# Optimization experiments

Hardware: AMD Instinct MI355X
Metric: run time of the kernel (lower is better)

The kernel has to match this reference:

```python
import jax, jax.numpy as jnp
import numpy as np

IN, H, T = 40, 64, 301


def setup_inputs() -> dict:
    key = jax.random.key(0)
    ks = jax.random.split(key, 7)
    s_ih = 1.0 / np.sqrt(H)
    return {
        "x": jax.random.normal(ks[0], (4096, T, IN), dtype=jnp.float32),
        # PyTorch LSTM layout: gates stacked as [i, f, g, o] along first dim
        "w_ih": jax.random.uniform(ks[1], (4 * H, IN), jnp.float32, -s_ih, s_ih),
        "w_hh": jax.random.uniform(ks[2], (4 * H, H), jnp.float32, -s_ih, s_ih),
        "b_ih": jax.random.uniform(ks[3], (4 * H,), jnp.float32, -s_ih, s_ih),
        "b_hh": jax.random.uniform(ks[4], (4 * H,), jnp.float32, -s_ih, s_ih),
        "w_clf": jax.random.uniform(ks[5], (1, T * H), jnp.float32, -1.0 / np.sqrt(T * H), 1.0 / np.sqrt(T * H)),
        "b_clf": jax.random.uniform(ks[6], (1,), jnp.float32, -1.0 / np.sqrt(T * H), 1.0 / np.sqrt(T * H)),
    }


def _lstm(x, w_ih, w_hh, b_ih, b_hh):
    B = x.shape[0]
    # precompute input projections for all timesteps: [B, T, 4H] -> [T, B, 4H]
    xw = jnp.einsum("bti,gi->btg", x, w_ih) + b_ih + b_hh
    xw = jnp.transpose(xw, (1, 0, 2))

    def step(carry, xt):
        h, c = carry
        z = xt + h @ w_hh.T  # [B, 4H]
        i, f, g, o = jnp.split(z, 4, axis=-1)
        c = jax.nn.sigmoid(f) * c + jax.nn.sigmoid(i) * jnp.tanh(g)
        h = jax.nn.sigmoid(o) * jnp.tanh(c)
        return (h, c), h

    h0 = jnp.zeros((B, H), x.dtype)
    c0 = jnp.zeros((B, H), x.dtype)
    _, hs = jax.lax.scan(step, (h0, c0), xw)  # hs: [T, B, H]
    return jnp.transpose(hs, (1, 0, 2))  # [B, T, H]


def reference(x, w_ih, w_hh, b_ih, b_hh, w_clf, b_clf):
    out = _lstm(x, w_ih, w_hh, b_ih, b_hh)  # [B, T, H]
    flat = out.reshape(out.shape[0], -1)  # [B, T*H]
    return flat @ w_clf.T + b_clf  # [B, 1]
```

## Files before the change

### kernel.cpp

```cpp
#include <hip/hip_runtime.h>

#define T_STEPS 301
#define IN_DIM  40
#define LOG2E   1.44269504088896340736f

typedef __attribute__((ext_vector_type(8))) _Float16 f16x8;
typedef __attribute__((ext_vector_type(4))) float f32x4;
typedef unsigned short ushort_t;
typedef unsigned int uint_t;

__device__ __forceinline__ f16x8 cvt8h(const float4 a, const float4 b) {
  f16x8 r;
  r[0] = (_Float16)a.x; r[1] = (_Float16)a.y; r[2] = (_Float16)a.z; r[3] = (_Float16)a.w;
  r[4] = (_Float16)b.x; r[5] = (_Float16)b.y; r[6] = (_Float16)b.z; r[7] = (_Float16)b.w;
  return r;
}

__device__ __forceinline__ float lstm_act(float zi, float zf, float zg, float zo, float& cc) {
  const float ig = __builtin_amdgcn_rcpf(1.0f + __builtin_amdgcn_exp2f(-zi));
  const float fg = __builtin_amdgcn_rcpf(1.0f + __builtin_amdgcn_exp2f(-zf));
  const float gg = 1.0f - 2.0f * __builtin_amdgcn_rcpf(1.0f + __builtin_amdgcn_exp2f(zg));
  const float og = __builtin_amdgcn_rcpf(1.0f + __builtin_amdgcn_exp2f(-zo));
  cc = fg * cc + ig * gg;
  const float tc = 1.0f - 2.0f * __builtin_amdgcn_rcpf(1.0f + __builtin_amdgcn_exp2f(cc * (2.0f * LOG2E)));
  return og * tc;
}

__global__ __launch_bounds__(256, 2)
void lstm_f16(const float* __restrict__ x, const float* __restrict__ w_ih,
              const float* __restrict__ w_hh, const float* __restrict__ b_ih,
              const float* __restrict__ b_hh, const float* __restrict__ w_clf,
              const float* __restrict__ b_clf, float* __restrict__ out) {
  __shared__ ushort_t hbuf[2][16][64];
  __shared__ float red[64][9];

  const int tid  = threadIdx.x;
  const int l    = tid & 63;
  const int w    = tid >> 6;
  const int arow = l & 15;
  const int g16  = l >> 4;
  const int n    = w * 16 + arow;

  const float gscale[4] = {LOG2E, LOG2E, 2.0f * LOG2E, LOG2E};

  f16x8 whh[4][2], wih[4][2];
  float biasv[4];
#pragma unroll
  for (int c = 0; c < 4; ++c) {
    const float s = gscale[c];
    const float* wr = w_hh + (size_t)(c * 64 + n) * 64;
#pragma unroll
    for (int kc = 0; kc < 2; ++kc) {
      float4 v0 = *(const float4*)(wr + kc * 32 + g16 * 8);
      float4 v1 = *(const float4*)(wr + kc * 32 + g16 * 8 + 4);
      v0.x *= s; v0.y *= s; v0.z *= s; v0.w *= s;
      v1.x *= s; v1.y *= s; v1.z *= s; v1.w *= s;
      whh[c][kc] = cvt8h(v0, v1);
    }
    const float* wir = w_ih + (size_t)(c * 64 + n) * IN_DIM;
    {
      float4 v0 = *(const float4*)(wir + g16 * 8);
      float4 v1 = *(const float4*)(wir + g16 * 8 + 4);
      v0.x *= s; v0.y *= s; v0.z *= s; v0.w *= s;
      v1.x *= s; v1.y *= s; v1.z *= s; v1.w *= s;
      wih[c][0] = cvt8h(v0, v1);
    }
    {
      float4 v0 = make_float4(0, 0, 0, 0), v1 = make_float4(0, 0, 0, 0);
      if (g16 == 0) {
        v0 = *(const float4*)(wir + 32);
        v1 = *(const float4*)(wir + 36);
        v0.x *= s; v0.y *= s; v0.z *= s; v0.w *= s;
        v1.x *= s; v1.y *= s; v1.z *= s; v1.w *= s;
      }
      wih[c][1] = cvt8h(v0, v1);
    }
    biasv[c] = (b_ih[c * 64 + n] + b_hh[c * 64 + n]) * s;
  }

  {
    uint_t* hz = (uint_t*)&hbuf[0][0][0];
    for (int i = tid; i < 1024; i += 256) hz[i] = 0;
  }
  __syncthreads();

  const int slot = ((arow >> 2) << 1) | (arow & 1);
  const int toff = (arow >> 1) & 1;
  const int gb   = blockIdx.x * 8 + slot;
  const float* xbase = x + (size_t)gb * T_STEPS * IN_DIM;

  float4 xa0, xa1, xb0 = make_float4(0, 0, 0, 0), xb1 = make_float4(0, 0, 0, 0);
  {
    const int tm = toff < T_STEPS ? toff : T_STEPS - 1;
    const float* xp = xbase + tm * IN_DIM + g16 * 8;
    xa0 = *(const float4*)xp;
    xa1 = *(const float4*)(xp + 4);
    if (g16 == 0) {
      xb0 = *(const float4*)(xbase + tm * IN_DIM + 32);
      xb1 = *(const float4*)(xbase + tm * IN_DIM + 36);
    }
  }

  f32x4 zacc[4];
  float cc0 = 0.f, cc1 = 0.f, a0 = 0.f, a1 = 0.f;
  float wc_cur = w_clf[n];

  const int row0 = g16 * 4, row1 = row0 + 1;
  const int wo0 = row0 * 64 + ((((n >> 3) ^ (row0 & 7)) << 3) | (n & 7));
  const int wo1 = row1 * 64 + ((((n >> 3) ^ (row1 & 7)) << 3) | (n & 7));
  ushort_t* hflat = &hbuf[0][0][0];

  for (int t = 0; t < T_STEPS; ++t) {
    const int rb = t & 1, wb = rb ^ 1;

    f16x8 ah0, ah1;
    {
      const int cj0 = g16 ^ (arow & 7);
      const int cj1 = (4 + g16) ^ (arow & 7);
      ah0 = *(const f16x8*)&hbuf[rb][arow][cj0 * 8];
      ah1 = *(const f16x8*)&hbuf[rb][arow][cj1 * 8];
    }

    f32x4 zcur[4];
    if ((t & 1) == 0) {
      const f16x8 xf0 = cvt8h(xa0, xa1);
      const f16x8 xf1 = cvt8h(xb0, xb1);
#pragma unroll
      for (int c = 0; c < 4; ++c) {
        zacc[c] = (f32x4){biasv[c], biasv[c], biasv[c], biasv[c]};
        zacc[c] = __builtin_amdgcn_mfma_f32_16x16x32_f16(xf0, wih[c][0], zacc[c], 0, 0, 0);
        zacc[c] = __builtin_amdgcn_mfma_f32_16x16x32_f16(xf1, wih[c][1], zacc[c], 0, 0, 0);
      }
      if (t + 2 < T_STEPS) {
        const int tm = (t + 2 + toff < T_STEPS) ? t + 2 + toff : T_STEPS - 1;
        const float* xp = xbase + tm * IN_DIM + g16 * 8;
        xa0 = *(const float4*)xp;
        xa1 = *(const float4*)(xp + 4);
        if (g16 == 0) {
          xb0 = *(const float4*)(xbase + tm * IN_DIM + 32);
          xb1 = *(const float4*)(xbase + tm * IN_DIM + 36);
        }
      }
#pragma unroll
      for (int c = 0; c < 4; ++c) {
        zacc[c] = __builtin_amdgcn_mfma_f32_16x16x32_f16(ah0, whh[c][0], zacc[c], 0, 0, 0);
        zacc[c] = __builtin_amdgcn_mfma_f32_16x16x32_f16(ah1, whh[c][1], zacc[c], 0, 0, 0);
        zcur[c] = zacc[c];
      }
    } else {
#pragma unroll
      for (int c = 0; c < 4; ++c) {
        f32x4 acc = __builtin_shufflevector(zacc[c], zacc[c], 2, 3, 2, 3);
        acc = __builtin_amdgcn_mfma_f32_16x16x32_f16(ah0, whh[c][0], acc, 0, 0, 0);
        acc = __builtin_amdgcn_mfma_f32_16x16x32_f16(ah1, whh[c][1], acc, 0, 0, 0);
        zcur[c] = acc;
      }
    }

    const float wcn = (t + 1 < T_STEPS) ? w_clf[(t + 1) * 64 + n] : wc_cur;

    const float h0 = lstm_act(zcur[0][0], zcur[1][0], zcur[2][0], zcur[3][0], cc0);
    const float h1 = lstm_act(zcur[0][1], zcur[1][1], zcur[2][1], zcur[3][1], cc1);
    a0 += h0 * wc_cur;
    a1 += h1 * wc_cur;
    wc_cur = wcn;

    {
      union { _Float16 h; ushort_t u; } u0, u1;
      u0.h = (_Float16)h0;
      u1.h = (_Float16)h1;
      ushort_t* hb = hflat + wb * 1024;
      hb[wo0] = u0.u;
      hb[wo1] = u1.u;
    }
    asm volatile("s_waitcnt lgkmcnt(0)\n\ts_barrier" ::: "memory");
  }

  red[n][g16 * 2 + 0] = a0;
  red[n][g16 * 2 + 1] = a1;
  __syncthreads();
  if (tid < 8) {
    float s = b_clf[0];
#pragma unroll 8
    for (int j = 0; j < 64; ++j) s += red[j][tid];
    out[blockIdx.x * 8 + tid] = s;
  }
}

extern "C" void kernel_launch(void* const* d_in, const int* in_sizes, int n_in,
                              void* d_out, int out_size, void* d_ws, size_t ws_size,
                              hipStream_t stream) {
  const float* x     = (const float*)d_in[0];
  const float* w_ih  = (const float*)d_in[1];
  const float* w_hh  = (const float*)d_in[2];
  const float* b_ih  = (const float*)d_in[3];
  const float* b_hh  = (const float*)d_in[4];
  const float* w_clf = (const float*)d_in[5];
  const float* b_clf = (const float*)d_in[6];
  float* out = (float*)d_out;

  lstm_f16<<<512, 256, 0, stream>>>(x, w_ih, w_hh, b_ih, b_hh, w_clf, b_clf, out);
}
```

Baseline: 190.8 us.

## Process 4 batch rows per block with 4-step unrolled shifted-row MFMA recurrence

Each block now handles 4 sequences instead of 8, and the grid doubles to 1024 blocks with launch bounds raised to 4 blocks per SM. The MFMA 16-row A tile is reused so each sequence occupies 4 rows offset by timestep: the input projection is computed once per 4 steps and the accumulator carries forward, with h written into shifted rows and stale rows zeroed. This gives each thread one h value per step instead of two, raising occupancy and cutting the activation work per thread. The trade-off is a fixed MFMA cost per step at lower useful density, plus more complex row bookkeeping; correctness depends on the zero-row trick and the swizzle being removed consistently.

```diff
diff --git a/kernel.cpp b/kernel.cpp
--- a/kernel.cpp
+++ b/kernel.cpp
@@ -26,20 +26,20 @@
   return og * tc;
 }
 
-__global__ __launch_bounds__(256, 2)
-void lstm_f16(const float* __restrict__ x, const float* __restrict__ w_ih,
-              const float* __restrict__ w_hh, const float* __restrict__ b_ih,
-              const float* __restrict__ b_hh, const float* __restrict__ w_clf,
-              const float* __restrict__ b_clf, float* __restrict__ out) {
+__global__ __launch_bounds__(256, 4)
+void lstm_q4(const float* __restrict__ x, const float* __restrict__ w_ih,
+             const float* __restrict__ w_hh, const float* __restrict__ b_ih,
+             const float* __restrict__ b_hh, const float* __restrict__ w_clf,
+             const float* __restrict__ b_clf, float* __restrict__ out) {
   __shared__ ushort_t hbuf[2][16][64];
-  __shared__ float red[64][9];
-
-  const int tid  = threadIdx.x;
-  const int l    = tid & 63;
-  const int w    = tid >> 6;
-  const int arow = l & 15;
-  const int g16  = l >> 4;
-  const int n    = w * 16 + arow;
+  __shared__ float red[64][5];
+
+  const int tid = threadIdx.x;
+  const int l   = tid & 63;
+  const int w   = tid >> 6;
+  const int r15 = l & 15;
+  const int g16 = l >> 4;
+  const int n   = w * 16 + r15;
 
   const float gscale[4] = {LOG2E, LOG2E, 2.0f * LOG2E, LOG2E};
 
@@ -84,45 +84,55 @@
   }
   __syncthreads();
 
-  const int slot = ((arow >> 2) << 1) | (arow & 1);
-  const int toff = (arow >> 1) & 1;
-  const int gb   = blockIdx.x * 8 + slot;
-  const float* xbase = x + (size_t)gb * T_STEPS * IN_DIM;
+  const int s_a = r15 >> 2;
+  const int q_a = r15 & 3;
+  const float* xbase = x + (size_t)(blockIdx.x * 4 + s_a) * T_STEPS * IN_DIM;
 
   float4 xa0, xa1, xb0 = make_float4(0, 0, 0, 0), xb1 = make_float4(0, 0, 0, 0);
   {
-    const int tm = toff < T_STEPS ? toff : T_STEPS - 1;
-    const float* xp = xbase + tm * IN_DIM + g16 * 8;
+    const float* xp = xbase + q_a * IN_DIM + g16 * 8;
     xa0 = *(const float4*)xp;
     xa1 = *(const float4*)(xp + 4);
     if (g16 == 0) {
-      xb0 = *(const float4*)(xbase + tm * IN_DIM + 32);
-      xb1 = *(const float4*)(xbase + tm * IN_DIM + 36);
+      xb0 = *(const float4*)(xbase + q_a * IN_DIM + 32);
+      xb1 = *(const float4*)(xbase + q_a * IN_DIM + 36);
     }
   }
 
   f32x4 zacc[4];
-  float cc0 = 0.f, cc1 = 0.f, a0 = 0.f, a1 = 0.f;
+  float cc = 0.f, a = 0.f;
   float wc_cur = w_clf[n];
-
-  const int row0 = g16 * 4, row1 = row0 + 1;
-  const int wo0 = row0 * 64 + ((((n >> 3) ^ (row0 & 7)) << 3) | (n & 7));
-  const int wo1 = row1 * 64 + ((((n >> 3) ^ (row1 & 7)) << 3) | (n & 7));
-  ushort_t* hflat = &hbuf[0][0][0];
-
-  for (int t = 0; t < T_STEPS; ++t) {
-    const int rb = t & 1, wb = rb ^ 1;
-
-    f16x8 ah0, ah1;
+  const int wrb = g16 * 4;
+
+  ushort_t* const rd0 = &hbuf[0][r15][g16 * 8];
+  ushort_t* const rd1 = &hbuf[1][r15][g16 * 8];
+
+#define QSTEP(Q, RB, WB, WROW, ZROW)                                              \
+  {                                                                               \
+    const int t = t0 + Q;                                                         \
+    f16x8 ah0 = *(const f16x8*)(RB);                                              \
+    f16x8 ah1 = *(const f16x8*)((RB) + 32);                                       \
+    _Pragma("unroll")                                                             \
+    for (int c = 0; c < 4; ++c) {                                                 \
+      zacc[c] = __builtin_amdgcn_mfma_f32_16x16x32_f16(ah0, whh[c][0], zacc[c], 0, 0, 0); \
+      zacc[c] = __builtin_amdgcn_mfma_f32_16x16x32_f16(ah1, whh[c][1], zacc[c], 0, 0, 0); \
+    }                                                                             \
+    const float wcn = (t + 1 < T_STEPS) ? w_clf[(t + 1) * 64 + n] : wc_cur;       \
+    const float h = lstm_act(zacc[0][Q], zacc[1][Q], zacc[2][Q], zacc[3][Q], cc); \
+    a += h * wc_cur;                                                              \
+    wc_cur = wcn;                                                                 \
+    union { _Float16 hf; ushort_t u; } cv;                                        \
+    cv.hf = (_Float16)h;                                                          \
+    hbuf[WB][wrb + WROW][n] = cv.u;                                               \
+    hbuf[WB][wrb + ZROW][n] = 0;                                                  \
+    asm volatile("s_waitcnt lgkmcnt(0)\n\ts_barrier" ::: "memory");               \
+  }
+
+  for (int p = 0; p <= 75; ++p) {
+    const int t0 = 4 * p;
     {
-      const int cj0 = g16 ^ (arow & 7);
-      const int cj1 = (4 + g16) ^ (arow & 7);
-      ah0 = *(const f16x8*)&hbuf[rb][arow][cj0 * 8];
-      ah1 = *(const f16x8*)&hbuf[rb][arow][cj1 * 8];
-    }
-
-    f32x4 zcur[4];
-    if ((t & 1) == 0) {
+      f16x8 ah0 = *(const f16x8*)(rd0);
+      f16x8 ah1 = *(const f16x8*)(rd0 + 32);
       const f16x8 xf0 = cvt8h(xa0, xa1);
       const f16x8 xf1 = cvt8h(xb0, xb1);
 #pragma unroll
@@ -131,8 +141,9 @@
         zacc[c] = __builtin_amdgcn_mfma_f32_16x16x32_f16(xf0, wih[c][0], zacc[c], 0, 0, 0);
         zacc[c] = __builtin_amdgcn_mfma_f32_16x16x32_f16(xf1, wih[c][1], zacc[c], 0, 0, 0);
       }
-      if (t + 2 < T_STEPS) {
-        const int tm = (t + 2 + toff < T_STEPS) ? t + 2 + toff : T_STEPS - 1;
+      if (t0 + 4 < T_STEPS) {
+        const int tq = t0 + 4 + q_a;
+        const int tm = (tq <= T_STEPS - 1) ? tq : T_STEPS - 1;
         const float* xp = xbase + tm * IN_DIM + g16 * 8;
         xa0 = *(const float4*)xp;
         xa1 = *(const float4*)(xp + 4);
@@ -145,45 +156,31 @@
       for (int c = 0; c < 4; ++c) {
         zacc[c] = __builtin_amdgcn_mfma_f32_16x16x32_f16(ah0, whh[c][0], zacc[c], 0, 0, 0);
         zacc[c] = __builtin_amdgcn_mfma_f32_16x16x32_f16(ah1, whh[c][1], zacc[c], 0, 0, 0);
-        zcur[c] = zacc[c];
-      }
-    } else {
-#pragma unroll
-      for (int c = 0; c < 4; ++c) {
-        f32x4 acc = __builtin_shufflevector(zacc[c], zacc[c], 2, 3, 2, 3);
-        acc = __builtin_amdgcn_mfma_f32_16x16x32_f16(ah0, whh[c][0], acc, 0, 0, 0);
-        acc = __builtin_amdgcn_mfma_f32_16x16x32_f16(ah1, whh[c][1], acc, 0, 0, 0);
-        zcur[c] = acc;
-      }
-    }
-
-    const float wcn = (t + 1 < T_STEPS) ? w_clf[(t + 1) * 64 + n] : wc_cur;
-
-    const float h0 = lstm_act(zcur[0][0], zcur[1][0], zcur[2][0], zcur[3][0], cc0);
-    const float h1 = lstm_act(zcur[0][1], zcur[1][1], zcur[2][1], zcur[3][1], cc1);
-    a0 += h0 * wc_cur;
-    a1 += h1 * wc_cur;
-    wc_cur = wcn;
-
-    {
-      union { _Float16 h; ushort_t u; } u0, u1;
-      u0.h = (_Float16)h0;
-      u1.h = (_Float16)h1;
-      ushort_t* hb = hflat + wb * 1024;
-      hb[wo0] = u0.u;
-      hb[wo1] = u1.u;
-    }
-    asm volatile("s_waitcnt lgkmcnt(0)\n\ts_barrier" ::: "memory");
-  }
-
-  red[n][g16 * 2 + 0] = a0;
-  red[n][g16 * 2 + 1] = a1;
+      }
+      const float wcn = (t0 + 1 < T_STEPS) ? w_clf[(t0 + 1) * 64 + n] : wc_cur;
+      const float h = lstm_act(zacc[0][0], zacc[1][0], zacc[2][0], zacc[3][0], cc);
+      a += h * wc_cur;
+      wc_cur = wcn;
+      union { _Float16 hf; ushort_t u; } cv;
+      cv.hf = (_Float16)h;
+      hbuf[1][wrb + 1][n] = cv.u;
+      hbuf[1][wrb + 3][n] = 0;
+      if (t0 + 1 >= T_STEPS) break;
+      asm volatile("s_waitcnt lgkmcnt(0)\n\ts_barrier" ::: "memory");
+    }
+    QSTEP(1, rd1, 0, 2, 0)
+    QSTEP(2, rd0, 1, 3, 1)
+    QSTEP(3, rd1, 0, 0, 2)
+  }
+#undef QSTEP
+
+  red[n][g16] = a;
   __syncthreads();
-  if (tid < 8) {
+  if (tid < 4) {
     float s = b_clf[0];
 #pragma unroll 8
     for (int j = 0; j < 64; ++j) s += red[j][tid];
-    out[blockIdx.x * 8 + tid] = s;
+    out[blockIdx.x * 4 + tid] = s;
   }
 }
 
@@ -199,5 +196,5 @@
   const float* b_clf = (const float*)d_in[6];
   float* out = (float*)d_out;
 
-  lstm_f16<<<512, 256, 0, stream>>>(x, w_ih, w_hh, b_ih, b_hh, w_clf, b_clf, out);
-}
+  lstm_q4<<<1024, 256, 0, stream>>>(x, w_ih, w_hh, b_ih, b_hh, w_clf, b_clf, out);
+}
```

New measurement: 302.4 us. 58.5% more time.
